# Performance work log

Hardware: AMD Instinct MI355X
Metric: run time of the kernel (lower is better)

## Reference

```python
import jax, jax.numpy as jnp
import numpy as np

B, S, E, H, FF = 8, 1024, 1024, 16, 4096
DK = E // H
EPS = 1.1920929e-07  # torch RMSNorm default eps = finfo(float32).eps


def _rmsnorm(x, g):
    return x * jax.lax.rsqrt(jnp.mean(x * x, axis=-1, keepdims=True) + EPS) * g


def _rope(q, k):
    # q, k: [B, H, S, DK]; standard rotate-half RoPE, theta=10000
    d = q.shape[-1]
    s = q.shape[-2]
    inv_freq = 1.0 / (10000.0 ** (jnp.arange(0, d, 2, dtype=jnp.float32) / d))
    ang = jnp.arange(s, dtype=jnp.float32)[:, None] * inv_freq  # [S, d/2]
    cos = jnp.concatenate([jnp.cos(ang), jnp.cos(ang)], axis=-1)  # [S, d]
    sin = jnp.concatenate([jnp.sin(ang), jnp.sin(ang)], axis=-1)

    def rot(x):
        x1, x2 = jnp.split(x, 2, axis=-1)
        return jnp.concatenate([-x2, x1], axis=-1)

    return q * cos + rot(q) * sin, k * cos + rot(k) * sin


def setup_inputs() -> dict:
    key = jax.random.key(0)
    ks = jax.random.split(key, 16)
    sc = 0.02
    inp = {
        "x": jax.random.normal(ks[0], (B, S, E), dtype=jnp.float32),
        "WQ": jax.random.normal(ks[1], (E, E), dtype=jnp.float32) * sc,
        "bQ": jnp.zeros((E,), jnp.float32),
        "WK": jax.random.normal(ks[2], (E, E), dtype=jnp.float32) * sc,
        "bK": jnp.zeros((E,), jnp.float32),
        "WV": jax.random.normal(ks[3], (E, E), dtype=jnp.float32) * sc,
        "bV": jnp.zeros((E,), jnp.float32),
        "WO": jax.random.normal(ks[4], (E, E), dtype=jnp.float32) * sc,
        "bO": jnp.zeros((E,), jnp.float32),
        "W1": jax.random.normal(ks[5], (E, FF), dtype=jnp.float32) * sc,
        "b1": jnp.zeros((FF,), jnp.float32),
        "W2": jax.random.normal(ks[6], (FF, E), dtype=jnp.float32) * sc,
        "b2": jnp.zeros((E,), jnp.float32),
        "g1": jnp.ones((E,), jnp.float32),
        "g2": jnp.ones((E,), jnp.float32),
    }
    return inp


def reference(x, WQ, bQ, WK, bK, WV, bV, WO, bO, W1, b1, W2, b2, g1, g2):
    b, s, e = x.shape

    def attn(h):
        q = (h @ WQ + bQ).reshape(b, s, H, DK).transpose(0, 2, 1, 3)
        k = (h @ WK + bK).reshape(b, s, H, DK).transpose(0, 2, 1, 3)
        v = (h @ WV + bV).reshape(b, s, H, DK).transpose(0, 2, 1, 3)
        q, k = _rope(q, k)
        scores = jnp.einsum("bhqd,bhkd->bhqk", q, k) / jnp.sqrt(jnp.float32(DK))
        p = jax.nn.softmax(scores, axis=-1)
        o = jnp.einsum("bhqk,bhkd->bhqd", p, v)
        o = o.transpose(0, 2, 1, 3).reshape(b, s, e)
        return o @ WO + bO

    def ffn(h):
        return jax.nn.relu(h @ W1 + b1) @ W2 + b2

    x = x + attn(_rmsnorm(x, g1))
    x = x + ffn(_rmsnorm(x, g2))
    return x
```

## Files before the change

### kernel.cpp

```cpp
#include <hip/hip_runtime.h>
#include <math.h>

#define B_ 8
#define S_ 1024
#define E_ 1024
#define H_ 16
#define FF_ 4096

typedef __attribute__((ext_vector_type(8))) short bf16x8;
typedef __attribute__((ext_vector_type(4))) float f32x4;

#define QSCALE 0.1803368801111f
#define LG2_10K 0.4152410118f

__device__ __forceinline__ unsigned short f2bf(float f) {
  union { float f; unsigned u; } v;
  v.f = f;
  unsigned r = v.u + 0x7fffu + ((v.u >> 16) & 1u);
  return (unsigned short)(r >> 16);
}
__device__ __forceinline__ float bf2f(unsigned short u) {
  union { unsigned u; float f; } v;
  v.u = ((unsigned)u) << 16;
  return v.f;
}
__device__ __forceinline__ unsigned fbits(float f) {
  union { float f; unsigned u; } v;
  v.f = f;
  return v.u;
}

__device__ __forceinline__ void glds16(const void* g, void* l) {
  __builtin_amdgcn_global_load_lds(
      (const __attribute__((address_space(1))) unsigned int*)g,
      (__attribute__((address_space(3))) unsigned int*)l, 16, 0, 0);
}

__global__ __launch_bounds__(256) void wconvT(const float* __restrict__ W,
                                              unsigned short* __restrict__ Wt,
                                              int K, int N) {
  __shared__ float t[32][33];
  const int tx = threadIdx.x & 31, ty = threadIdx.x >> 5;
  const int n0 = blockIdx.x * 32, k0 = blockIdx.y * 32;
#pragma unroll
  for (int p = 0; p < 4; ++p)
    t[ty + p * 8][tx] = W[(size_t)(k0 + ty + p * 8) * N + n0 + tx];
  __syncthreads();
#pragma unroll
  for (int p = 0; p < 4; ++p)
    Wt[(size_t)(n0 + ty + p * 8) * K + k0 + tx] = f2bf(t[tx][ty + p * 8]);
}

__global__ __launch_bounds__(256) void bpack(const float* __restrict__ bQ,
                                             const float* __restrict__ bK,
                                             const float* __restrict__ bV,
                                             float* __restrict__ o) {
  const int i = blockIdx.x * 256 + threadIdx.x;
  const float v = (i < 1024) ? bQ[i] : ((i < 2048) ? bK[i - 1024] : bV[i - 2048]);
  o[i] = v;
}

__global__ __launch_bounds__(256) void rmsnorm_kernel(const float* __restrict__ x,
                                                      const float* __restrict__ g,
                                                      unsigned short* __restrict__ out) {
  const int row = blockIdx.x;
  const int t = threadIdx.x;
  const float4 v = ((const float4*)(x + (size_t)row * E_))[t];
  float ss = v.x * v.x + v.y * v.y + v.z * v.z + v.w * v.w;
#pragma unroll
  for (int off = 32; off > 0; off >>= 1) ss += __shfl_down(ss, off);
  __shared__ float sred[4];
  if ((t & 63) == 0) sred[t >> 6] = ss;
  __syncthreads();
  const float tot = sred[0] + sred[1] + sred[2] + sred[3];
  const float rinv = rsqrtf(tot * (1.0f / E_) + 1.1920929e-07f);
  const float4 gv = ((const float4*)g)[t];
  ushort4 o;
  o.x = f2bf(v.x * rinv * gv.x);
  o.y = f2bf(v.y * rinv * gv.y);
  o.z = f2bf(v.z * rinv * gv.z);
  o.w = f2bf(v.w * rinv * gv.w);
  ((ushort4*)(out + (size_t)row * E_))[t] = o;
}

template <int OUT_BF16, int RELU, int RES>
__global__ __launch_bounds__(256) void gemm_bf16(const unsigned short* __restrict__ A,
                                                 const unsigned short* __restrict__ Bt,
                                                 const float* __restrict__ bias,
                                                 const float* __restrict__ res,
                                                 void* __restrict__ C,
                                                 int M, int N, int K) {
  __shared__ unsigned short As[128 * 32];
  __shared__ unsigned short Bs[128 * 32];
  const int tid = threadIdx.x;
  const int w = tid >> 6;
  const int lane = tid & 63;

  const int nb = gridDim.x;
  const int id = blockIdx.x;
  const int lid = (id & 7) * (nb >> 3) + (id >> 3);
  const int per = (M >> 7) * 8;
  const int grp = lid / per;
  const int rem = lid - grp * per;
  const int bn = (grp * 8 + (rem & 7)) * 128;
  const int bm = (rem >> 3) * 128;

  const int wm = (w & 1) * 64, wn = (w >> 1) * 64;

  f32x4 acc[4][4];
#pragma unroll
  for (int i = 0; i < 4; ++i)
#pragma unroll
    for (int j = 0; j < 4; ++j) acc[i][j] = (f32x4){0.f, 0.f, 0.f, 0.f};

  const unsigned short* Ap0 = A + (size_t)(bm + w * 32 + (lane >> 2)) * K + (lane & 3) * 8;
  const unsigned short* Ap1 = Ap0 + (size_t)16 * K;
  const unsigned short* Bp0 = Bt + (size_t)(bn + w * 32 + (lane >> 2)) * K + (lane & 3) * 8;
  const unsigned short* Bp1 = Bp0 + (size_t)16 * K;
  unsigned short* AsD0 = &As[w * 1024];
  unsigned short* AsD1 = AsD0 + 512;
  unsigned short* BsD0 = &Bs[w * 1024];
  unsigned short* BsD1 = BsD0 + 512;

  const int fr = lane & 15;
  const int fk = (lane >> 4) * 8;

  for (int k0 = 0; k0 < K; k0 += 32) {
    __syncthreads();
    glds16(Ap0 + k0, AsD0);
    glds16(Ap1 + k0, AsD1);
    glds16(Bp0 + k0, BsD0);
    glds16(Bp1 + k0, BsD1);
    __syncthreads();
    bf16x8 a[4], b[4];
#pragma unroll
    for (int im = 0; im < 4; ++im)
      a[im] = *(const bf16x8*)&As[(wm + im * 16 + fr) * 32 + fk];
#pragma unroll
    for (int in = 0; in < 4; ++in)
      b[in] = *(const bf16x8*)&Bs[(wn + in * 16 + fr) * 32 + fk];
#pragma unroll
    for (int im = 0; im < 4; ++im)
#pragma unroll
      for (int in = 0; in < 4; ++in)
        acc[im][in] = __builtin_amdgcn_mfma_f32_16x16x32_bf16(a[im], b[in], acc[im][in], 0, 0, 0);
  }

#pragma unroll
  for (int im = 0; im < 4; ++im) {
    const int row0 = bm + wm + im * 16 + (lane >> 4) * 4;
#pragma unroll
    for (int in = 0; in < 4; ++in) {
      const int col = bn + wn + in * 16 + (lane & 15);
      const float bv = bias[col];
#pragma unroll
      for (int r = 0; r < 4; ++r) {
        float v = acc[im][in][r] + bv;
        if (RES) v += res[(size_t)(row0 + r) * N + col];
        if (RELU) v = fmaxf(v, 0.0f);
        if (OUT_BF16)
          ((unsigned short*)C)[(size_t)(row0 + r) * N + col] = f2bf(v);
        else
          ((float*)C)[(size_t)(row0 + r) * N + col] = v;
      }
    }
  }
}

template <int OUT_BF16, int RELU, int RES>
__global__ __launch_bounds__(256) void gemm_n64(const unsigned short* __restrict__ A,
                                                const unsigned short* __restrict__ Bt,
                                                const float* __restrict__ bias,
                                                const float* __restrict__ res,
                                                void* __restrict__ C,
                                                int M, int N, int K) {
  __shared__ unsigned short As[128 * 32];
  __shared__ unsigned short Bs[64 * 32];
  const int tid = threadIdx.x;
  const int w = tid >> 6;
  const int lane = tid & 63;

  const int nbn = N >> 6;
  const int bm = (blockIdx.x / nbn) * 128;
  const int bn = (blockIdx.x % nbn) * 64;

  const int wm = (w & 1) * 64, wn = (w >> 1) * 32;

  f32x4 acc[4][2];
#pragma unroll
  for (int i = 0; i < 4; ++i)
#pragma unroll
    for (int j = 0; j < 2; ++j) acc[i][j] = (f32x4){0.f, 0.f, 0.f, 0.f};

  const unsigned short* Ap0 = A + (size_t)(bm + w * 32 + (lane >> 2)) * K + (lane & 3) * 8;
  const unsigned short* Ap1 = Ap0 + (size_t)16 * K;
  const unsigned short* Bp0 = Bt + (size_t)(bn + w * 16 + (lane >> 2)) * K + (lane & 3) * 8;
  unsigned short* AsD0 = &As[w * 1024];
  unsigned short* AsD1 = AsD0 + 512;
  unsigned short* BsD0 = &Bs[w * 512];

  const int fr = lane & 15;
  const int fk = (lane >> 4) * 8;

  for (int k0 = 0; k0 < K; k0 += 32) {
    __syncthreads();
    glds16(Ap0 + k0, AsD0);
    glds16(Ap1 + k0, AsD1);
    glds16(Bp0 + k0, BsD0);
    __syncthreads();
    bf16x8 a[4], b[2];
#pragma unroll
    for (int im = 0; im < 4; ++im)
      a[im] = *(const bf16x8*)&As[(wm + im * 16 + fr) * 32 + fk];
#pragma unroll
    for (int in = 0; in < 2; ++in)
      b[in] = *(const bf16x8*)&Bs[(wn + in * 16 + fr) * 32 + fk];
#pragma unroll
    for (int im = 0; im < 4; ++im)
#pragma unroll
      for (int in = 0; in < 2; ++in)
        acc[im][in] = __builtin_amdgcn_mfma_f32_16x16x32_bf16(a[im], b[in], acc[im][in], 0, 0, 0);
  }

#pragma unroll
  for (int im = 0; im < 4; ++im) {
    const int row0 = bm + wm + im * 16 + (lane >> 4) * 4;
#pragma unroll
    for (int in = 0; in < 2; ++in) {
      const int col = bn + wn + in * 16 + fr;
      const float bv = bias[col];
#pragma unroll
      for (int r = 0; r < 4; ++r) {
        float v = acc[im][in][r] + bv;
        if (RES) v += res[(size_t)(row0 + r) * N + col];
        if (RELU) v = fmaxf(v, 0.0f);
        if (OUT_BF16)
          ((unsigned short*)C)[(size_t)(row0 + r) * N + col] = f2bf(v);
        else
          ((float*)C)[(size_t)(row0 + r) * N + col] = v;
      }
    }
  }
}

__global__ __launch_bounds__(256) void gemm_qkv(const unsigned short* __restrict__ A,
                                                const unsigned short* __restrict__ Bt,
                                                const float* __restrict__ bias,
                                                unsigned short* __restrict__ QKV,
                                                unsigned short* __restrict__ Vt,
                                                int M, int K) {
  const int N = 3072;
  __shared__ unsigned short As[128 * 32];
  __shared__ unsigned short Bs[128 * 32];
  const int tid = threadIdx.x;
  const int w = tid >> 6;
  const int lane = tid & 63;

  const int nb = gridDim.x;
  const int id = blockIdx.x;
  const int lid = (id & 7) * (nb >> 3) + (id >> 3);
  const int per = (M >> 7) * 8;
  const int grp = lid / per;
  const int rem = lid - grp * per;
  const int bn = (grp * 8 + (rem & 7)) * 128;
  const int bm = (rem >> 3) * 128;

  const int wm = (w & 1) * 64, wn = (w >> 1) * 64;

  f32x4 acc[4][4];
#pragma unroll
  for (int i = 0; i < 4; ++i)
#pragma unroll
    for (int j = 0; j < 4; ++j) acc[i][j] = (f32x4){0.f, 0.f, 0.f, 0.f};

  const unsigned short* Ap0 = A + (size_t)(bm + w * 32 + (lane >> 2)) * K + (lane & 3) * 8;
  const unsigned short* Ap1 = Ap0 + (size_t)16 * K;
  const unsigned short* Bp0 = Bt + (size_t)(bn + w * 32 + (lane >> 2)) * K + (lane & 3) * 8;
  const unsigned short* Bp1 = Bp0 + (size_t)16 * K;
  unsigned short* AsD0 = &As[w * 1024];
  unsigned short* AsD1 = AsD0 + 512;
  unsigned short* BsD0 = &Bs[w * 1024];
  unsigned short* BsD1 = BsD0 + 512;

  const int fr = lane & 15;
  const int fk = (lane >> 4) * 8;

  for (int k0 = 0; k0 < K; k0 += 32) {
    __syncthreads();
    glds16(Ap0 + k0, AsD0);
    glds16(Ap1 + k0, AsD1);
    glds16(Bp0 + k0, BsD0);
    glds16(Bp1 + k0, BsD1);
    __syncthreads();
    bf16x8 a[4], b[4];
#pragma unroll
    for (int im = 0; im < 4; ++im)
      a[im] = *(const bf16x8*)&As[(wm + im * 16 + fr) * 32 + fk];
#pragma unroll
    for (int in = 0; in < 4; ++in)
      b[in] = *(const bf16x8*)&Bs[(wn + in * 16 + fr) * 32 + fk];
#pragma unroll
    for (int im = 0; im < 4; ++im)
#pragma unroll
      for (int in = 0; in < 4; ++in)
        acc[im][in] = __builtin_amdgcn_mfma_f32_16x16x32_bf16(a[im], b[in], acc[im][in], 0, 0, 0);
  }

  const int cbase = bn + wn;
  const int seg = cbase >> 6;
  const int typ = seg >> 4;
  const int hh = seg & 15;
  const int bidx = bm >> 10;
  float bv[4];
#pragma unroll
  for (int in = 0; in < 4; ++in) bv[in] = bias[cbase + in * 16 + fr];

  if (typ == 2) {
#pragma unroll
    for (int im = 0; im < 4; ++im) {
      const int s0 = (bm & 1023) + wm + im * 16 + (lane >> 4) * 4;
#pragma unroll
      for (int in = 0; in < 4; ++in) {
        const int d = in * 16 + fr;
        ushort4 o4;
        o4.x = f2bf(acc[im][in][0] + bv[in]);
        o4.y = f2bf(acc[im][in][1] + bv[in]);
        o4.z = f2bf(acc[im][in][2] + bv[in]);
        o4.w = f2bf(acc[im][in][3] + bv[in]);
        *(ushort4*)&Vt[(size_t)((bidx * 16 + hh) * 64 + d) * S_ + s0] = o4;
      }
    }
  } else {
    const float qs = (typ == 0) ? QSCALE : 1.0f;
    const float i0 = exp2f(-LG2_10K * (float)fr);
    const float i1 = exp2f(-LG2_10K * (float)(fr + 16));
#pragma unroll
    for (int im = 0; im < 4; ++im) {
      const int row0 = bm + wm + im * 16 + (lane >> 4) * 4;
#pragma unroll
      for (int r = 0; r < 4; ++r) {
        const int row = row0 + r;
        const float s = (float)(row & 1023);
        float sn0, cs0, sn1, cs1;
        __sincosf(s * i0, &sn0, &cs0);
        __sincosf(s * i1, &sn1, &cs1);
        const float x0 = acc[im][0][r] + bv[0];
        const float x1 = acc[im][1][r] + bv[1];
        const float x2 = acc[im][2][r] + bv[2];
        const float x3 = acc[im][3][r] + bv[3];
        unsigned short* cp = QKV + (size_t)row * 3072 + cbase;
        cp[fr]      = f2bf((x0 * cs0 - x2 * sn0) * qs);
        cp[16 + fr] = f2bf((x1 * cs1 - x3 * sn1) * qs);
        cp[32 + fr] = f2bf((x2 * cs0 + x0 * sn0) * qs);
        cp[48 + fr] = f2bf((x3 * cs1 + x1 * sn1) * qs);
      }
    }
  }
}

__global__ __launch_bounds__(256) void attn_v4(const unsigned short* __restrict__ QKV,
                                               const unsigned short* __restrict__ Vt,
                                               unsigned short* __restrict__ Og) {
  __shared__ unsigned short Kf[2][8 * 512];
  __shared__ unsigned short Vf[2][8 * 512];
  __shared__ unsigned short Ps[4][32 * 72];
  const int tid = threadIdx.x;
  const int w = tid >> 6, lane = tid & 63;
  const int qt = blockIdx.x, bh = blockIdx.y;
  const int b = bh >> 4, h = bh & 15;
  const int fr = lane & 15, g = lane >> 4, fk = g * 8;
  const int q0w = qt * 128 + w * 32;

  bf16x8 qB[2][2];
#pragma unroll
  for (int nt = 0; nt < 2; ++nt)
#pragma unroll
    for (int c = 0; c < 2; ++c)
      qB[nt][c] = *(const bf16x8*)&QKV[(size_t)(b * S_ + q0w + nt * 16 + fr) * 3072 +
                                       h * 64 + c * 32 + fk];

  f32x4 o[4][2];
#pragma unroll
  for (int mt = 0; mt < 4; ++mt)
#pragma unroll
    for (int nt = 0; nt < 2; ++nt) o[mt][nt] = (f32x4){0.f, 0.f, 0.f, 0.f};
  float l[2] = {0.0f, 0.0f};

#define STAGE(kt, bufi)                                                                   \
  {                                                                                       \
    _Pragma("unroll") for (int p = 0; p < 4; ++p) {                                       \
      const int u = w * 4 + p;                                                            \
      if (u < 8) {                                                                        \
        const int mt = u >> 1, c = u & 1;                                                 \
        glds16(QKV + (size_t)(b * S_ + (kt) * 64 + mt * 16 + fr) * 3072 + 1024 + h * 64 + \
                   c * 32 + fk,                                                           \
               &Kf[bufi][u * 512]);                                                       \
      } else {                                                                            \
        const int v2 = u - 8, mt = v2 >> 1, c = v2 & 1;                                   \
        glds16(Vt + (size_t)(bh * 64 + mt * 16 + fr) * S_ + (kt) * 64 + c * 32 + fk,      \
               &Vf[bufi][v2 * 512]);                                                      \
      }                                                                                   \
    }                                                                                     \
  }

  STAGE(0, 0);

  for (int kt = 0; kt < 16; ++kt) {
    __syncthreads();
    if (kt < 15) STAGE(kt + 1, (kt + 1) & 1);
    const unsigned short* Kc = Kf[kt & 1];
    const unsigned short* Vc = Vf[kt & 1];

    f32x4 s[4][2];
#pragma unroll
    for (int mt = 0; mt < 4; ++mt) {
      const bf16x8 k0 = *(const bf16x8*)&Kc[(mt * 2 + 0) * 512 + lane * 8];
      const bf16x8 k1 = *(const bf16x8*)&Kc[(mt * 2 + 1) * 512 + lane * 8];
#pragma unroll
      for (int nt = 0; nt < 2; ++nt) {
        f32x4 a = (f32x4){0.f, 0.f, 0.f, 0.f};
        a = __builtin_amdgcn_mfma_f32_16x16x32_bf16(k0, qB[nt][0], a, 0, 0, 0);
        a = __builtin_amdgcn_mfma_f32_16x16x32_bf16(k1, qB[nt][1], a, 0, 0, 0);
        s[mt][nt] = a;
      }
    }

#pragma unroll
    for (int nt = 0; nt < 2; ++nt) {
      float rs = 0.0f;
#pragma unroll
      for (int mt = 0; mt < 4; ++mt)
#pragma unroll
        for (int r = 0; r < 4; ++r) {
          const float p = exp2f(s[mt][nt][r]);
          s[mt][nt][r] = p;
          rs += p;
        }
      rs += __shfl_xor(rs, 16);
      rs += __shfl_xor(rs, 32);
      l[nt] += rs;
    }

#pragma unroll
    for (int nt = 0; nt < 2; ++nt)
#pragma unroll
      for (int mt = 0; mt < 4; ++mt) {
        uint2 pk;
        pk.x = __builtin_amdgcn_perm(fbits(s[mt][nt][1]), fbits(s[mt][nt][0]), 0x07060302u);
        pk.y = __builtin_amdgcn_perm(fbits(s[mt][nt][3]), fbits(s[mt][nt][2]), 0x07060302u);
        *(uint2*)&Ps[w][(nt * 16 + fr) * 72 + mt * 16 + g * 4] = pk;
      }

    bf16x8 pB[2][2];
#pragma unroll
    for (int nt = 0; nt < 2; ++nt)
#pragma unroll
      for (int c = 0; c < 2; ++c)
        pB[nt][c] = *(const bf16x8*)&Ps[w][(nt * 16 + fr) * 72 + c * 32 + fk];
#pragma unroll
    for (int mt = 0; mt < 4; ++mt) {
      const bf16x8 v0 = *(const bf16x8*)&Vc[(mt * 2 + 0) * 512 + lane * 8];
      const bf16x8 v1 = *(const bf16x8*)&Vc[(mt * 2 + 1) * 512 + lane * 8];
#pragma unroll
      for (int nt = 0; nt < 2; ++nt) {
        o[mt][nt] = __builtin_amdgcn_mfma_f32_16x16x32_bf16(v0, pB[nt][0], o[mt][nt], 0, 0, 0);
        o[mt][nt] = __builtin_amdgcn_mfma_f32_16x16x32_bf16(v1, pB[nt][1], o[mt][nt], 0, 0, 0);
      }
    }
  }

  const float linv0 = 1.0f / l[0], linv1 = 1.0f / l[1];
#pragma unroll
  for (int nt = 0; nt < 2; ++nt) {
    const float li = nt ? linv1 : linv0;
#pragma unroll
    for (int mt = 0; mt < 4; ++mt) {
      uint2 pk;
      pk.x = __builtin_amdgcn_perm(fbits(o[mt][nt][1] * li), fbits(o[mt][nt][0] * li), 0x07060302u);
      pk.y = __builtin_amdgcn_perm(fbits(o[mt][nt][3] * li), fbits(o[mt][nt][2] * li), 0x07060302u);
      *(uint2*)&Ps[w][(nt * 16 + fr) * 72 + mt * 16 + g * 4] = pk;
    }
  }
  const int qr = lane >> 1, hf = lane & 1;
#pragma unroll
  for (int c = 0; c < 2; ++c) {
    const bf16x8 vv = *(const bf16x8*)&Ps[w][qr * 72 + hf * 16 + c * 32];
    *(bf16x8*)&Og[(size_t)(b * S_ + q0w + qr) * E_ + h * 64 + hf * 16 + c * 32] = vv;
  }
}

extern "C" void kernel_launch(void* const* d_in, const int* in_sizes, int n_in,
                              void* d_out, int out_size, void* d_ws, size_t ws_size,
                              hipStream_t stream) {
  const float* x  = (const float*)d_in[0];
  const float* WQ = (const float*)d_in[1];
  const float* bQ = (const float*)d_in[2];
  const float* WK = (const float*)d_in[3];
  const float* bK = (const float*)d_in[4];
  const float* WV = (const float*)d_in[5];
  const float* bV = (const float*)d_in[6];
  const float* WO = (const float*)d_in[7];
  const float* bO = (const float*)d_in[8];
  const float* W1 = (const float*)d_in[9];
  const float* b1 = (const float*)d_in[10];
  const float* W2 = (const float*)d_in[11];
  const float* b2 = (const float*)d_in[12];
  const float* g1 = (const float*)d_in[13];
  const float* g2 = (const float*)d_in[14];
  float* out = (float*)d_out;

  char* ws = (char*)d_ws;
  const size_t MB = 1024 * 1024;
  unsigned short* h1   = (unsigned short*)(ws + 0 * MB);
  unsigned short* QKV  = (unsigned short*)(ws + 16 * MB);
  unsigned short* Vt   = (unsigned short*)(ws + 64 * MB);
  unsigned short* Ob   = (unsigned short*)(ws + 80 * MB);
  float*          x1   = (float*)(ws + 96 * MB);
  unsigned short* h2   = (unsigned short*)(ws + 128 * MB);
  unsigned short* mid  = (unsigned short*)(ws + 16 * MB);
  unsigned short* WQKVt= (unsigned short*)(ws + 144 * MB);
  unsigned short* WOt  = (unsigned short*)(ws + 150 * MB);
  unsigned short* W1t  = (unsigned short*)(ws + 152 * MB);
  unsigned short* W2t  = (unsigned short*)(ws + 160 * MB);
  float*          bqkv = (float*)(ws + 168 * MB);

  const int M = B_ * S_;

  wconvT<<<dim3(32, 32), 256, 0, stream>>>(WQ, WQKVt, E_, E_);
  wconvT<<<dim3(32, 32), 256, 0, stream>>>(WK, WQKVt + 1024 * 1024, E_, E_);
  wconvT<<<dim3(32, 32), 256, 0, stream>>>(WV, WQKVt + 2 * 1024 * 1024, E_, E_);
  wconvT<<<dim3(32, 32), 256, 0, stream>>>(WO, WOt, E_, E_);
  wconvT<<<dim3(128, 32), 256, 0, stream>>>(W1, W1t, E_, FF_);
  wconvT<<<dim3(32, 128), 256, 0, stream>>>(W2, W2t, FF_, E_);
  bpack<<<12, 256, 0, stream>>>(bQ, bK, bV, bqkv);

  rmsnorm_kernel<<<M, 256, 0, stream>>>(x, g1, h1);

  gemm_qkv<<<24 * 64, 256, 0, stream>>>(h1, WQKVt, bqkv, QKV, Vt, M, E_);

  attn_v4<<<dim3(8, B_ * H_), 256, 0, stream>>>(QKV, Vt, Ob);

  gemm_n64<0, 0, 1><<<64 * 16, 256, 0, stream>>>(Ob, WOt, bO, x, x1, M, E_, E_);

  rmsnorm_kernel<<<M, 256, 0, stream>>>(x1, g2, h2);

  gemm_bf16<1, 1, 0><<<32 * 64, 256, 0, stream>>>(h2, W1t, b1, nullptr, mid, M, FF_, E_);

  gemm_n64<0, 0, 1><<<64 * 16, 256, 0, stream>>>(mid, W2t, b2, x1, out, M, E_, FF_);
}
```

Before: 542.8 us.

## Split-K the FFN down-projection with 128x128 tiles and a separate reduce

Replaces the 128x64-tile FF2 GEMM with a two-way split-K kernel that uses 128x128 tiles and writes bf16 partial sums. A separate elementwise kernel then adds the partials, the bias and the residual. It also merges the four square weight transpose/convert launches into one 3D-grid launch. The larger tiles improve data reuse and keep the block count at 1024, but the change adds partial-sum traffic, an extra launch, and bf16 rounding of the partials.

```diff
diff --git a/kernel.cpp b/kernel.cpp
--- a/kernel.cpp
+++ b/kernel.cpp
@@ -49,6 +49,29 @@
 #pragma unroll
   for (int p = 0; p < 4; ++p)
     Wt[(size_t)(n0 + ty + p * 8) * K + k0 + tx] = f2bf(t[tx][ty + p * 8]);
+}
+
+__global__ __launch_bounds__(256) void wconvT4(const float* __restrict__ W0,
+                                               const float* __restrict__ W1p,
+                                               const float* __restrict__ W2p,
+                                               const float* __restrict__ W3p,
+                                               unsigned short* __restrict__ D0,
+                                               unsigned short* __restrict__ D1,
+                                               unsigned short* __restrict__ D2,
+                                               unsigned short* __restrict__ D3) {
+  __shared__ float t[32][33];
+  const int z = blockIdx.z;
+  const float* W = (z == 0) ? W0 : (z == 1) ? W1p : (z == 2) ? W2p : W3p;
+  unsigned short* D = (z == 0) ? D0 : (z == 1) ? D1 : (z == 2) ? D2 : D3;
+  const int tx = threadIdx.x & 31, ty = threadIdx.x >> 5;
+  const int n0 = blockIdx.x * 32, k0 = blockIdx.y * 32;
+#pragma unroll
+  for (int p = 0; p < 4; ++p)
+    t[ty + p * 8][tx] = W[(size_t)(k0 + ty + p * 8) * E_ + n0 + tx];
+  __syncthreads();
+#pragma unroll
+  for (int p = 0; p < 4; ++p)
+    D[(size_t)(n0 + ty + p * 8) * E_ + k0 + tx] = f2bf(t[tx][ty + p * 8]);
 }
 
 __global__ __launch_bounds__(256) void bpack(const float* __restrict__ bQ,
@@ -165,6 +188,98 @@
       }
     }
   }
+}
+
+__global__ __launch_bounds__(256) void gemm_sk2(const unsigned short* __restrict__ A,
+                                                const unsigned short* __restrict__ Bt,
+                                                unsigned short* __restrict__ Pp) {
+  const int N = 1024, K = 4096, KH = 2048;
+  __shared__ unsigned short As[128 * 32];
+  __shared__ unsigned short Bs[128 * 32];
+  const int tid = threadIdx.x;
+  const int w = tid >> 6;
+  const int lane = tid & 63;
+
+  const int id = blockIdx.x;
+  const int kh = id >> 9;
+  const int hid = id & 511;
+  const int lid = (hid & 7) * 64 + (hid >> 3);
+  const int bn = (lid & 7) * 128;
+  const int bm = (lid >> 3) * 128;
+
+  const int wm = (w & 1) * 64, wn = (w >> 1) * 64;
+
+  f32x4 acc[4][4];
+#pragma unroll
+  for (int i = 0; i < 4; ++i)
+#pragma unroll
+    for (int j = 0; j < 4; ++j) acc[i][j] = (f32x4){0.f, 0.f, 0.f, 0.f};
+
+  const unsigned short* Ap0 =
+      A + (size_t)(bm + w * 32 + (lane >> 2)) * K + kh * KH + (lane & 3) * 8;
+  const unsigned short* Ap1 = Ap0 + (size_t)16 * K;
+  const unsigned short* Bp0 =
+      Bt + (size_t)(bn + w * 32 + (lane >> 2)) * K + kh * KH + (lane & 3) * 8;
+  const unsigned short* Bp1 = Bp0 + (size_t)16 * K;
+  unsigned short* AsD0 = &As[w * 1024];
+  unsigned short* AsD1 = AsD0 + 512;
+  unsigned short* BsD0 = &Bs[w * 1024];
+  unsigned short* BsD1 = BsD0 + 512;
+
+  const int fr = lane & 15;
+  const int fk = (lane >> 4) * 8;
+
+  for (int k0 = 0; k0 < KH; k0 += 32) {
+    __syncthreads();
+    glds16(Ap0 + k0, AsD0);
+    glds16(Ap1 + k0, AsD1);
+    glds16(Bp0 + k0, BsD0);
+    glds16(Bp1 + k0, BsD1);
+    __syncthreads();
+    bf16x8 a[4], b[4];
+#pragma unroll
+    for (int im = 0; im < 4; ++im)
+      a[im] = *(const bf16x8*)&As[(wm + im * 16 + fr) * 32 + fk];
+#pragma unroll
+    for (int in = 0; in < 4; ++in)
+      b[in] = *(const bf16x8*)&Bs[(wn + in * 16 + fr) * 32 + fk];
+#pragma unroll
+    for (int im = 0; im < 4; ++im)
+#pragma unroll
+      for (int in = 0; in < 4; ++in)
+        acc[im][in] = __builtin_amdgcn_mfma_f32_16x16x32_bf16(a[im], b[in], acc[im][in], 0, 0, 0);
+  }
+
+  unsigned short* P = Pp + (size_t)kh * (8u << 20);
+#pragma unroll
+  for (int im = 0; im < 4; ++im) {
+    const int row0 = bm + wm + im * 16 + (lane >> 4) * 4;
+#pragma unroll
+    for (int in = 0; in < 4; ++in) {
+      const int col = bn + wn + in * 16 + fr;
+#pragma unroll
+      for (int r = 0; r < 4; ++r)
+        P[(size_t)(row0 + r) * N + col] = f2bf(acc[im][in][r]);
+    }
+  }
+}
+
+__global__ __launch_bounds__(256) void ff2_reduce(const unsigned short* __restrict__ Pp,
+                                                  const float* __restrict__ x1,
+                                                  const float* __restrict__ b2,
+                                                  float* __restrict__ out) {
+  const int i = blockIdx.x * 256 + threadIdx.x;
+  const size_t off = (size_t)i * 4;
+  const ushort4 p0 = *(const ushort4*)(Pp + off);
+  const ushort4 p1 = *(const ushort4*)(Pp + (8u << 20) + off);
+  const float4 xv = *(const float4*)(x1 + off);
+  const float4 bv = *(const float4*)(b2 + (off & 1023));
+  float4 o;
+  o.x = xv.x + bv.x + bf2f(p0.x) + bf2f(p1.x);
+  o.y = xv.y + bv.y + bf2f(p0.y) + bf2f(p1.y);
+  o.z = xv.z + bv.z + bf2f(p0.z) + bf2f(p1.z);
+  o.w = xv.w + bv.w + bf2f(p0.w) + bf2f(p1.w);
+  *(float4*)(out + off) = o;
 }
 
 template <int OUT_BF16, int RELU, int RES>
@@ -523,13 +638,13 @@
   unsigned short* W1t  = (unsigned short*)(ws + 152 * MB);
   unsigned short* W2t  = (unsigned short*)(ws + 160 * MB);
   float*          bqkv = (float*)(ws + 168 * MB);
+  unsigned short* Pp   = (unsigned short*)(ws + 176 * MB);
 
   const int M = B_ * S_;
 
-  wconvT<<<dim3(32, 32), 256, 0, stream>>>(WQ, WQKVt, E_, E_);
-  wconvT<<<dim3(32, 32), 256, 0, stream>>>(WK, WQKVt + 1024 * 1024, E_, E_);
-  wconvT<<<dim3(32, 32), 256, 0, stream>>>(WV, WQKVt + 2 * 1024 * 1024, E_, E_);
-  wconvT<<<dim3(32, 32), 256, 0, stream>>>(WO, WOt, E_, E_);
+  wconvT4<<<dim3(32, 32, 4), 256, 0, stream>>>(WQ, WK, WV, WO, WQKVt,
+                                               WQKVt + 1024 * 1024,
+                                               WQKVt + 2 * 1024 * 1024, WOt);
   wconvT<<<dim3(128, 32), 256, 0, stream>>>(W1, W1t, E_, FF_);
   wconvT<<<dim3(32, 128), 256, 0, stream>>>(W2, W2t, FF_, E_);
   bpack<<<12, 256, 0, stream>>>(bQ, bK, bV, bqkv);
@@ -546,5 +661,7 @@
 
   gemm_bf16<1, 1, 0><<<32 * 64, 256, 0, stream>>>(h2, W1t, b1, nullptr, mid, M, FF_, E_);
 
-  gemm_n64<0, 0, 1><<<64 * 16, 256, 0, stream>>>(mid, W2t, b2, x1, out, M, E_, FF_);
-}
+  gemm_sk2<<<1024, 256, 0, stream>>>(mid, W2t, Pp);
+
+  ff2_reduce<<<8192, 256, 0, stream>>>(Pp, x1, b2, out);
+}
```

Result: no change. 537.7 us (-0.9%).
